# Kernel optimization log

Measured on AMD Instinct MI355X. Metric: run time of the kernel, lower is better.

## Reference

```python
import jax, jax.numpy as jnp
import numpy as np
from jax import lax

B_, L_, D_ = 4, 2048, 256
DI, NS, DC, DTR = 512, 16, 4, 16  # d_inner=2*D, d_state, d_conv, dt_rank=ceil(D/16)
DFF = 4 * D_


def setup_inputs():
    key = jax.random.key(0)
    ks = jax.random.split(key, 20)
    rn = lambda k, s, sc=0.02: jax.random.normal(k, s, jnp.float32) * sc
    return {
        "x": jax.random.normal(ks[0], (B_, L_, D_), jnp.float32),
        "in_proj_w": rn(ks[1], (2 * DI, D_)), "in_proj_b": jnp.zeros((2 * DI,), jnp.float32),
        "conv_w": rn(ks[2], (DI, DC), 0.1), "conv_b": jnp.zeros((DI,), jnp.float32),
        "x_proj_w": rn(ks[3], (DTR + 2 * NS, DI)),
        "dt_proj_w": rn(ks[4], (DI, DTR), 0.1), "dt_proj_b": rn(ks[5], (DI,), 0.5),
        "A_log": jnp.log(jnp.tile(jnp.arange(1, NS + 1, dtype=jnp.float32), (DI, 1))),
        "D_ssm": jnp.ones((DI,), jnp.float32),
        "out_proj_w": rn(ks[6], (D_, DI)), "out_proj_b": jnp.zeros((D_,), jnp.float32),
        "ln1_g": jnp.ones((D_,), jnp.float32), "ln1_b": jnp.zeros((D_,), jnp.float32),
        "fc1_w": rn(ks[7], (DFF, D_)), "fc1_b": jnp.zeros((DFF,), jnp.float32),
        "fc2_w": rn(ks[8], (D_, DFF)), "fc2_b": jnp.zeros((D_,), jnp.float32),
        "ln2_g": jnp.ones((D_,), jnp.float32), "ln2_b": jnp.zeros((D_,), jnp.float32),
    }


def _layer_norm(x, g, b, eps=1e-5):
    m = jnp.mean(x, -1, keepdims=True)
    v = jnp.mean((x - m) ** 2, -1, keepdims=True)
    return (x - m) / jnp.sqrt(v + eps) * g + b


def _mamba(x, in_proj_w, in_proj_b, conv_w, conv_b, x_proj_w, dt_proj_w, dt_proj_b, A_log, D_ssm, out_proj_w, out_proj_b):
    B, L, D = x.shape
    xz = x @ in_proj_w.T + in_proj_b                       # [B,L,2*DI]
    xi, z = jnp.split(xz, 2, axis=-1)
    # causal depthwise conv over time
    xc = jnp.transpose(xi, (0, 2, 1))                       # [B,DI,L]
    xc = lax.conv_general_dilated(xc, conv_w[:, None, :], (1,), [(DC - 1, 0)],
                                  dimension_numbers=("NCH", "OIH", "NCH"),
                                  feature_group_count=DI)
    xi = jax.nn.silu(jnp.transpose(xc + conv_b[None, :, None], (0, 2, 1)))  # [B,L,DI]
    x_dbl = xi @ x_proj_w.T                                 # [B,L,DTR+2*NS]
    dt, Bs, Cs = jnp.split(x_dbl, [DTR, DTR + NS], axis=-1)
    dt = jax.nn.softplus(dt @ dt_proj_w.T + dt_proj_b)      # [B,L,DI]
    A = -jnp.exp(A_log)                                     # [DI,NS]
    dA = jnp.exp(dt[..., None] * A)                         # [B,L,DI,NS]
    dBu = dt[..., None] * Bs[:, :, None, :] * xi[..., None]  # [B,L,DI,NS]
    dA_t = jnp.moveaxis(dA, 1, 0)
    dBu_t = jnp.moveaxis(dBu, 1, 0)
    C_t = jnp.moveaxis(Cs, 1, 0)                            # [L,B,NS]

    def step(h, inp):
        a, bu, c = inp
        h = a * h + bu                                      # [B,DI,NS]
        y = jnp.einsum("bdn,bn->bd", h, c)
        return h, y

    h0 = jnp.zeros((B, DI, NS), x.dtype)
    _, ys = lax.scan(step, h0, (dA_t, dBu_t, C_t))
    y = jnp.moveaxis(ys, 0, 1) + xi * D_ssm                 # [B,L,DI]
    y = y * jax.nn.silu(z)
    return y @ out_proj_w.T + out_proj_b


def reference(x, in_proj_w, in_proj_b, conv_w, conv_b, x_proj_w, dt_proj_w, dt_proj_b,
              A_log, D_ssm, out_proj_w, out_proj_b, ln1_g, ln1_b, fc1_w, fc1_b,
              fc2_w, fc2_b, ln2_g, ln2_b):
    gelu = lambda t: jax.nn.gelu(t, approximate=False)
    ssm = _mamba(x, in_proj_w, in_proj_b, conv_w, conv_b, x_proj_w, dt_proj_w,
                 dt_proj_b, A_log, D_ssm, out_proj_w, out_proj_b)
    y = _layer_norm(x + ssm, ln1_g, ln1_b)                  # dropout = identity (eval)
    ffn = gelu(gelu(y @ fc1_w.T + fc1_b) @ fc2_w.T + fc2_b)
    return _layer_norm(y + ffn, ln2_g, ln2_b)
```

## Files before the change

kernel.cpp:

```cpp
#include <hip/hip_runtime.h>

typedef __bf16 bf16x8 __attribute__((ext_vector_type(8)));
typedef float  f32x4  __attribute__((ext_vector_type(4)));

#define AS1 __attribute__((address_space(1)))
#define AS3 __attribute__((address_space(3)))

__device__ __forceinline__ float bf2f(ushort u) {
    union { unsigned int i; float f; } v; v.i = ((unsigned int)u) << 16; return v.f;
}
__device__ __forceinline__ ushort f2bf(float f) {
    union { float f; unsigned int i; } v; v.f = f;
    unsigned int i = v.i;
    unsigned int r = i + 0x7FFFu + ((i >> 16) & 1u);
    return (ushort)(r >> 16);
}
__device__ __forceinline__ float bflo(unsigned int u) { return bf2f((ushort)(u & 0xFFFFu)); }
__device__ __forceinline__ float bfhi(unsigned int u) { return bf2f((ushort)(u >> 16)); }
__device__ __forceinline__ float gelu_f(float v) {
    return 0.5f * v * (1.f + erff(v * 0.70710678118654752f));
}

__device__ __forceinline__ bool sniff_inline(const ushort* __restrict__ x) {
    const int lane = threadIdx.x & 63;
    int cnt = 0;
    #pragma unroll
    for (int r = 0; r < 4; r++) {
        const ushort u = x[lane + r * 64];
        const int e = (u >> 7) & 0xFF;
        if ((u & 0x7FFF) == 0 || (e >= 112 && e <= 141)) cnt++;
    }
    #pragma unroll
    for (int o = 32; o > 0; o >>= 1) cnt += __shfl_xor(cnt, o);
    return cnt >= 224;
}

struct CanonArgs {
    const void* src[20];
    int off[20];
    int total;
};

__launch_bounds__(256)
__global__ void canon_k(CanonArgs a, ushort* __restrict__ dst, ushort* __restrict__ xpw_pad,
                        const ushort* __restrict__ sniffx)
{
    const int i = blockIdx.x * 256 + threadIdx.x;
    if (i >= a.total) {
        const int j = i - a.total;
        if (j < 8192) xpw_pad[24576 + j] = 0;
        return;
    }
    const bool fl = sniff_inline(sniffx);
    int s = 0;
    #pragma unroll
    for (int t = 1; t < 20; t++) if (i >= a.off[t]) s = t;
    const int li = i - a.off[s];
    ushort v;
    if (fl) v = ((const ushort*)a.src[s])[li];
    else    v = f2bf(((const float*)a.src[s])[li]);
    dst[i] = v;
    if (s == 5) xpw_pad[li] = v;
}

template<int BM, int BN>
__launch_bounds__(256, 2)
__global__ void gemm_bt(const ushort* __restrict__ A, const ushort* __restrict__ W,
                        const ushort* __restrict__ bias, ushort* __restrict__ Cb,
                        int N, int K)
{
    constexpr int WMT = BM / 32;
    constexpr int WNT = BN / 32;
    __shared__ __align__(16) ushort As[BM * 32];
    __shared__ __align__(16) ushort Bs[BN * 32];
    const int tid  = threadIdx.x;
    const int wave = tid >> 6;
    const int lane = tid & 63;
    const int m0 = blockIdx.x * BM;
    const int n0 = blockIdx.y * BN;
    const int wm = (wave >> 1) * (BM / 2);
    const int wn = (wave & 1) * (BN / 2);
    const int lrow = lane & 15;
    const int quad = lane >> 4;

    f32x4 acc[WMT][WNT];
    #pragma unroll
    for (int i = 0; i < WMT; i++)
        #pragma unroll
        for (int j = 0; j < WNT; j++)
            #pragma unroll
            for (int r = 0; r < 4; r++) acc[i][j][r] = 0.f;

    for (int k0 = 0; k0 < K; k0 += 32) {
        #pragma unroll
        for (int t = 0; t < BM / 64; t++) {
            const int inst = t * 4 + wave;
            const int row  = inst * 16 + (lane >> 2);
            const int sub  = lane & 3;
            const ushort* gp = A + (size_t)(m0 + row) * K + (k0 + sub * 8);
            __builtin_amdgcn_global_load_lds((AS1 void*)(void*)gp,
                                             (AS3 void*)(As + inst * 512), 16, 0, 0);
        }
        #pragma unroll
        for (int t = 0; t < BN / 64; t++) {
            const int inst = t * 4 + wave;
            const int row  = inst * 16 + (lane >> 2);
            const int sub  = lane & 3;
            const ushort* gp = W + (size_t)(n0 + row) * K + (k0 + sub * 8);
            __builtin_amdgcn_global_load_lds((AS1 void*)(void*)gp,
                                             (AS3 void*)(Bs + inst * 512), 16, 0, 0);
        }
        __syncthreads();
        bf16x8 afr[WMT], bfr[WNT];
        #pragma unroll
        for (int i = 0; i < WMT; i++)
            afr[i] = *(const bf16x8*)&As[(wm + i * 16 + lrow) * 32 + quad * 8];
        #pragma unroll
        for (int j = 0; j < WNT; j++)
            bfr[j] = *(const bf16x8*)&Bs[(wn + j * 16 + lrow) * 32 + quad * 8];
        #pragma unroll
        for (int i = 0; i < WMT; i++)
            #pragma unroll
            for (int j = 0; j < WNT; j++)
                acc[i][j] = __builtin_amdgcn_mfma_f32_16x16x32_bf16(afr[i], bfr[j], acc[i][j], 0, 0, 0);
        __syncthreads();
    }

    #pragma unroll
    for (int i = 0; i < WMT; i++) {
        const int gm = m0 + wm + i * 16 + quad * 4;
        #pragma unroll
        for (int j = 0; j < WNT; j++) {
            const int gn = n0 + wn + j * 16 + lrow;
            const float bv = bf2f(bias[gn]);
            #pragma unroll
            for (int r = 0; r < 4; r++)
                Cb[(size_t)(gm + r) * N + gn] = f2bf(acc[i][j][r] + bv);
        }
    }
}

__launch_bounds__(512)
__global__ void convscan1_k(const ushort* __restrict__ xz, const ushort* __restrict__ cw,
                            const ushort* __restrict__ cb, const ushort* __restrict__ xpw_pad,
                            const ushort* __restrict__ dtw, const ushort* __restrict__ dtb,
                            const ushort* __restrict__ Alog,
                            float* __restrict__ xdbl, float* __restrict__ summ)
{
    __shared__ __align__(16) ushort xcs[32 * 520];
    __shared__ float XD[32 * 48];
    const int tid  = threadIdx.x;
    const int wave = tid >> 6;
    const int lane = tid & 63;
    const int lrow = lane & 15;
    const int quad = lane >> 4;
    const int c = blockIdx.x, b = blockIdx.y;
    const int t0 = b * 2048 + c * 32;

    {
        const int d8 = (tid & 63) * 8;
        ushort wl[32];
        *(uint4*)&wl[0]  = *(const uint4*)&cw[d8 * 4];
        *(uint4*)&wl[8]  = *(const uint4*)&cw[d8 * 4 + 8];
        *(uint4*)&wl[16] = *(const uint4*)&cw[d8 * 4 + 16];
        *(uint4*)&wl[24] = *(const uint4*)&cw[d8 * 4 + 24];
        ushort bl[8];
        *(uint4*)&bl[0] = *(const uint4*)&cb[d8];
        #pragma unroll
        for (int it = 0; it < 4; it++) {
            const int trow = it * 8 + (tid >> 6);
            const int t = t0 + trow;
            const int l = t & 2047;
            float acc[8];
            #pragma unroll
            for (int j = 0; j < 8; j++) acc[j] = bf2f(bl[j]);
            #pragma unroll
            for (int k = 0; k < 4; k++) {
                const int ls = l - 3 + k;
                if (ls >= 0) {
                    ushort xl[8];
                    *(uint4*)&xl[0] = *(const uint4*)&xz[(size_t)(t - 3 + k) * 1024 + d8];
                    #pragma unroll
                    for (int j = 0; j < 8; j++) acc[j] += bf2f(xl[j]) * bf2f(wl[j * 4 + k]);
                }
            }
            ushort ol[8];
            #pragma unroll
            for (int j = 0; j < 8; j++) {
                const float s = acc[j] / (1.f + __expf(-acc[j]));
                ol[j] = f2bf(s);
            }
            *(uint4*)&xcs[trow * 520 + d8] = *(uint4*)&ol[0];
        }
    }
    __syncthreads();

    {
        const int mt = wave >> 2, nt = wave & 3;
        const ushort* bptr = xpw_pad + (size_t)(nt * 16 + lrow) * 512 + quad * 8;
        f32x4 acc = {0.f, 0.f, 0.f, 0.f};
        bf16x8 bn = *(const bf16x8*)bptr;
        for (int k0 = 0; k0 < 512; k0 += 32) {
            const bf16x8 bc = bn;
            if (k0 + 32 < 512) bn = *(const bf16x8*)(bptr + k0 + 32);
            const bf16x8 afr = *(const bf16x8*)&xcs[(mt * 16 + lrow) * 520 + k0 + quad * 8];
            acc = __builtin_amdgcn_mfma_f32_16x16x32_bf16(afr, bc, acc, 0, 0, 0);
        }
        const int col = nt * 16 + lrow;
        if (col < 48) {
            #pragma unroll
            for (int r = 0; r < 4; r++) {
                const int row = mt * 16 + quad * 4 + r;
                XD[row * 48 + col] = acc[r];
                xdbl[(size_t)(t0 + row) * 64 + col] = acc[r];
            }
        }
    }
    __syncthreads();

    {
        const int d = tid;
        const uint4 w0 = *(const uint4*)&dtw[d * 16];
        const uint4 w1 = *(const uint4*)&dtw[d * 16 + 8];
        const float wd[16] = { bflo(w0.x), bfhi(w0.x), bflo(w0.y), bfhi(w0.y),
                               bflo(w0.z), bfhi(w0.z), bflo(w0.w), bfhi(w0.w),
                               bflo(w1.x), bfhi(w1.x), bflo(w1.y), bfhi(w1.y),
                               bflo(w1.z), bfhi(w1.z), bflo(w1.w), bfhi(w1.w) };
        const float dtbv = bf2f(dtb[d]);
        float A[16], h[16];
        #pragma unroll
        for (int n = 0; n < 16; n++) {
            A[n] = -__expf(bf2f(Alog[d * 16 + n]));
            h[n] = 0.f;
        }
        float sdt = 0.f;
        for (int i = 0; i < 32; i++) {
            const float* Xr = &XD[i * 48];
            float s = dtbv;
            #pragma unroll
            for (int k = 0; k < 16; k++) s += Xr[k] * wd[k];
            const float dtv = (s > 15.f) ? s : __logf(1.f + __expf(s));
            const float xiv = bf2f(xcs[i * 520 + d]);
            const float dx = dtv * xiv;
            sdt += dtv;
            #pragma unroll
            for (int n = 0; n < 16; n++) {
                const float da = __expf(dtv * A[n]);
                h[n] = da * h[n] + dx * Xr[16 + n];
            }
        }
        const size_t base = ((size_t)(b * 64 + c) * 32) * 512 + d;
        #pragma unroll
        for (int n = 0; n < 16; n++) summ[base + (size_t)n * 512] = __expf(A[n] * sdt);
        #pragma unroll
        for (int n = 0; n < 16; n++) summ[base + (size_t)(16 + n) * 512] = h[n];
    }
}

__launch_bounds__(512)
__global__ void combine_k(float* __restrict__ summ)
{
    const int b = blockIdx.x >> 4, n = blockIdx.x & 15;
    const int d = threadIdx.x;
    float h = 0.f;
    #pragma unroll
    for (int half = 0; half < 2; half++) {
        float p[32], hl[32], ho[32];
        #pragma unroll
        for (int c2 = 0; c2 < 32; c2++) {
            const size_t sb = ((size_t)((b * 64 + half * 32 + c2) * 32 + n)) * 512 + d;
            p[c2]  = summ[sb];
            hl[c2] = summ[sb + 8192];
        }
        #pragma unroll
        for (int c2 = 0; c2 < 32; c2++) {
            ho[c2] = h;
            h = p[c2] * h + hl[c2];
        }
        #pragma unroll
        for (int c2 = 0; c2 < 32; c2++) {
            const size_t sb = ((size_t)((b * 64 + half * 32 + c2) * 32 + n)) * 512 + d;
            summ[sb] = ho[c2];
        }
    }
}

__launch_bounds__(512)
__global__ void tail_k(const ushort* __restrict__ xz, const ushort* __restrict__ cw,
                       const ushort* __restrict__ cb, const float* __restrict__ xdbl,
                       const ushort* __restrict__ dtw, const ushort* __restrict__ dtb,
                       const ushort* __restrict__ Alog, const float* __restrict__ summ,
                       const ushort* __restrict__ Dssm, const ushort* __restrict__ cx,
                       const ushort* __restrict__ opw, const ushort* __restrict__ opb,
                       const ushort* __restrict__ ln1g, const ushort* __restrict__ ln1b,
                       const ushort* __restrict__ f1w, const ushort* __restrict__ f1b,
                       const ushort* __restrict__ f2w, const ushort* __restrict__ f2b,
                       const ushort* __restrict__ ln2g, const ushort* __restrict__ ln2b,
                       void* __restrict__ dout, const ushort* __restrict__ sniffx)
{
    __shared__ __align__(16) ushort yls[32 * 520];
    __shared__ float XD[32 * 48];
    __shared__ __align__(16) ushort y1bs[32 * 264];
    __shared__ float redS[8 * 32], redQ[8 * 32];
    ushort* f1q = yls;

    const int tid  = threadIdx.x;
    const int wave = tid >> 6;
    const int lane = tid & 63;
    const int lrow = lane & 15;
    const int quad = lane >> 4;
    const int c = blockIdx.x, b = blockIdx.y;
    const int t0 = b * 2048 + c * 32;
    const int n0w = wave * 32;

    {
        const int d8 = (tid & 63) * 8;
        ushort wl[32];
        *(uint4*)&wl[0]  = *(const uint4*)&cw[d8 * 4];
        *(uint4*)&wl[8]  = *(const uint4*)&cw[d8 * 4 + 8];
        *(uint4*)&wl[16] = *(const uint4*)&cw[d8 * 4 + 16];
        *(uint4*)&wl[24] = *(const uint4*)&cw[d8 * 4 + 24];
        ushort bl[8];
        *(uint4*)&bl[0] = *(const uint4*)&cb[d8];
        #pragma unroll
        for (int it = 0; it < 4; it++) {
            const int trow = it * 8 + (tid >> 6);
            const int t = t0 + trow;
            const int l = t & 2047;
            float acc[8];
            #pragma unroll
            for (int j = 0; j < 8; j++) acc[j] = bf2f(bl[j]);
            #pragma unroll
            for (int k = 0; k < 4; k++) {
                const int ls = l - 3 + k;
                if (ls >= 0) {
                    ushort xl[8];
                    *(uint4*)&xl[0] = *(const uint4*)&xz[(size_t)(t - 3 + k) * 1024 + d8];
                    #pragma unroll
                    for (int j = 0; j < 8; j++) acc[j] += bf2f(xl[j]) * bf2f(wl[j * 4 + k]);
                }
            }
            ushort ol[8];
            #pragma unroll
            for (int j = 0; j < 8; j++) {
                const float s = acc[j] / (1.f + __expf(-acc[j]));
                ol[j] = f2bf(s);
            }
            *(uint4*)&yls[trow * 520 + d8] = *(uint4*)&ol[0];
        }
    }
    for (int e = tid; e < 1536; e += 512)
        XD[e] = xdbl[(size_t)(t0 + (e / 48)) * 64 + (e % 48)];
    __syncthreads();

    {
        const int d = tid;
        const uint4 w0 = *(const uint4*)&dtw[d * 16];
        const uint4 w1 = *(const uint4*)&dtw[d * 16 + 8];
        const float wd[16] = { bflo(w0.x), bfhi(w0.x), bflo(w0.y), bfhi(w0.y),
                               bflo(w0.z), bfhi(w0.z), bflo(w0.w), bfhi(w0.w),
                               bflo(w1.x), bfhi(w1.x), bflo(w1.y), bfhi(w1.y),
                               bflo(w1.z), bfhi(w1.z), bflo(w1.w), bfhi(w1.w) };
        const float dtbv = bf2f(dtb[d]);
        float A[16], h[16];
        #pragma unroll
        for (int n = 0; n < 16; n++) A[n] = -__expf(bf2f(Alog[d * 16 + n]));
        const size_t base = ((size_t)(b * 64 + c) * 32) * 512 + d;
        #pragma unroll
        for (int n = 0; n < 16; n++) h[n] = summ[base + (size_t)n * 512];
        const float Dv = bf2f(Dssm[d]);
        for (int i = 0; i < 32; i++) {
            const int t = t0 + i;
            const float* Xr = &XD[i * 48];
            float s = dtbv;
            #pragma unroll
            for (int k = 0; k < 16; k++) s += Xr[k] * wd[k];
            const float dtv = (s > 15.f) ? s : __logf(1.f + __expf(s));
            const float xiv = bf2f(yls[i * 520 + d]);
            const float dx = dtv * xiv;
            float yv = 0.f;
            #pragma unroll
            for (int n = 0; n < 16; n++) {
                const float da = __expf(dtv * A[n]);
                h[n] = da * h[n] + dx * Xr[16 + n];
                yv += h[n] * Xr[32 + n];
            }
            yv += xiv * Dv;
            const float zv = bf2f(xz[(size_t)t * 1024 + 512 + d]);
            yv *= zv / (1.f + __expf(-zv));
            yls[i * 520 + d] = f2bf(yv);
        }
    }
    __syncthreads();

    f32x4 accP[2][2];
    #pragma unroll
    for (int i = 0; i < 2; i++)
        #pragma unroll
        for (int j = 0; j < 2; j++)
            #pragma unroll
            for (int r = 0; r < 4; r++) accP[i][j][r] = 0.f;
    {
        const ushort* bp0 = opw + (size_t)(n0w + lrow) * 512 + quad * 8;
        const ushort* bp1 = opw + (size_t)(n0w + 16 + lrow) * 512 + quad * 8;
        bf16x8 bn0 = *(const bf16x8*)bp0;
        bf16x8 bn1 = *(const bf16x8*)bp1;
        for (int k0 = 0; k0 < 512; k0 += 32) {
            const bf16x8 bc0 = bn0, bc1 = bn1;
            if (k0 + 32 < 512) {
                bn0 = *(const bf16x8*)(bp0 + k0 + 32);
                bn1 = *(const bf16x8*)(bp1 + k0 + 32);
            }
            bf16x8 afr[2];
            #pragma unroll
            for (int i = 0; i < 2; i++)
                afr[i] = *(const bf16x8*)&yls[(i * 16 + lrow) * 520 + k0 + quad * 8];
            #pragma unroll
            for (int i = 0; i < 2; i++) {
                accP[i][0] = __builtin_amdgcn_mfma_f32_16x16x32_bf16(afr[i], bc0, accP[i][0], 0, 0, 0);
                accP[i][1] = __builtin_amdgcn_mfma_f32_16x16x32_bf16(afr[i], bc1, accP[i][1], 0, 0, 0);
            }
        }
    }
    float vP[2][2][4];
    float ps[2][4], pq[2][4];
    #pragma unroll
    for (int i = 0; i < 2; i++)
        #pragma unroll
        for (int r = 0; r < 4; r++) { ps[i][r] = 0.f; pq[i][r] = 0.f; }
    #pragma unroll
    for (int i = 0; i < 2; i++) {
        #pragma unroll
        for (int j = 0; j < 2; j++) {
            const int col = n0w + j * 16 + lrow;
            const float bv = bf2f(opb[col]);
            #pragma unroll
            for (int r = 0; r < 4; r++) {
                const int row = i * 16 + quad * 4 + r;
                float v = accP[i][j][r] + bv + bf2f(cx[(size_t)(t0 + row) * 256 + col]);
                vP[i][j][r] = v;
                ps[i][r] += v;
                pq[i][r] += v * v;
            }
        }
    }
    #pragma unroll
    for (int i = 0; i < 2; i++)
        #pragma unroll
        for (int r = 0; r < 4; r++) {
            #pragma unroll
            for (int o = 8; o > 0; o >>= 1) {
                ps[i][r] += __shfl_xor(ps[i][r], o);
                pq[i][r] += __shfl_xor(pq[i][r], o);
            }
            if (lrow == 0) {
                const int row = i * 16 + quad * 4 + r;
                redS[wave * 32 + row] = ps[i][r];
                redQ[wave * 32 + row] = pq[i][r];
            }
        }
    __syncthreads();

    float y1f[2][2][4];
    #pragma unroll
    for (int i = 0; i < 2; i++) {
        #pragma unroll
        for (int r = 0; r < 4; r++) {
            const int row = i * 16 + quad * 4 + r;
            float S = 0.f, Q = 0.f;
            #pragma unroll
            for (int w = 0; w < 8; w++) { S += redS[w * 32 + row]; Q += redQ[w * 32 + row]; }
            const float mean = S * (1.f / 256.f);
            const float var  = Q * (1.f / 256.f) - mean * mean;
            const float rs   = rsqrtf(var + 1e-5f);
            #pragma unroll
            for (int j = 0; j < 2; j++) {
                const int col = n0w + j * 16 + lrow;
                const float o2 = (vP[i][j][r] - mean) * rs * bf2f(ln1g[col]) + bf2f(ln1b[col]);
                y1f[i][j][r] = o2;
                y1bs[row * 264 + col] = f2bf(o2);
            }
        }
    }
    __syncthreads();

    f32x4 acc2[2][2];
    #pragma unroll
    for (int i = 0; i < 2; i++)
        #pragma unroll
        for (int j = 0; j < 2; j++)
            #pragma unroll
            for (int r = 0; r < 4; r++) acc2[i][j][r] = 0.f;

    for (int q = 0; q < 4; q++) {
        f32x4 a1[2][2];
        #pragma unroll
        for (int i = 0; i < 2; i++)
            #pragma unroll
            for (int j = 0; j < 2; j++)
                #pragma unroll
                for (int r = 0; r < 4; r++) a1[i][j][r] = 0.f;
        {
            const ushort* bp0 = f1w + (size_t)(q * 256 + n0w + lrow) * 256 + quad * 8;
            const ushort* bp1 = f1w + (size_t)(q * 256 + n0w + 16 + lrow) * 256 + quad * 8;
            bf16x8 bn0 = *(const bf16x8*)bp0;
            bf16x8 bn1 = *(const bf16x8*)bp1;
            for (int k0 = 0; k0 < 256; k0 += 32) {
                const bf16x8 bc0 = bn0, bc1 = bn1;
                if (k0 + 32 < 256) {
                    bn0 = *(const bf16x8*)(bp0 + k0 + 32);
                    bn1 = *(const bf16x8*)(bp1 + k0 + 32);
                }
                bf16x8 afr[2];
                #pragma unroll
                for (int i = 0; i < 2; i++)
                    afr[i] = *(const bf16x8*)&y1bs[(i * 16 + lrow) * 264 + k0 + quad * 8];
                #pragma unroll
                for (int i = 0; i < 2; i++) {
                    a1[i][0] = __builtin_amdgcn_mfma_f32_16x16x32_bf16(afr[i], bc0, a1[i][0], 0, 0, 0);
                    a1[i][1] = __builtin_amdgcn_mfma_f32_16x16x32_bf16(afr[i], bc1, a1[i][1], 0, 0, 0);
                }
            }
        }
        #pragma unroll
        for (int i = 0; i < 2; i++)
            #pragma unroll
            for (int j = 0; j < 2; j++) {
                const int qc = n0w + j * 16 + lrow;
                const float bv = bf2f(f1b[q * 256 + qc]);
                #pragma unroll
                for (int r = 0; r < 4; r++) {
                    const int row = i * 16 + quad * 4 + r;
                    f1q[row * 260 + qc] = f2bf(gelu_f(a1[i][j][r] + bv));
                }
            }
        __syncthreads();
        {
            const ushort* bp0 = f2w + (size_t)(n0w + lrow) * 1024 + q * 256 + quad * 8;
            const ushort* bp1 = f2w + (size_t)(n0w + 16 + lrow) * 1024 + q * 256 + quad * 8;
            bf16x8 bn0 = *(const bf16x8*)bp0;
            bf16x8 bn1 = *(const bf16x8*)bp1;
            for (int k0 = 0; k0 < 256; k0 += 32) {
                const bf16x8 bc0 = bn0, bc1 = bn1;
                if (k0 + 32 < 256) {
                    bn0 = *(const bf16x8*)(bp0 + k0 + 32);
                    bn1 = *(const bf16x8*)(bp1 + k0 + 32);
                }
                bf16x8 afr[2];
                #pragma unroll
                for (int i = 0; i < 2; i++)
                    afr[i] = *(const bf16x8*)&f1q[(i * 16 + lrow) * 260 + k0 + quad * 8];
                #pragma unroll
                for (int i = 0; i < 2; i++) {
                    acc2[i][0] = __builtin_amdgcn_mfma_f32_16x16x32_bf16(afr[i], bc0, acc2[i][0], 0, 0, 0);
                    acc2[i][1] = __builtin_amdgcn_mfma_f32_16x16x32_bf16(afr[i], bc1, acc2[i][1], 0, 0, 0);
                }
            }
        }
        __syncthreads();
    }

    float v2[2][2][4];
    #pragma unroll
    for (int i = 0; i < 2; i++)
        #pragma unroll
        for (int r = 0; r < 4; r++) { ps[i][r] = 0.f; pq[i][r] = 0.f; }
    #pragma unroll
    for (int i = 0; i < 2; i++)
        #pragma unroll
        for (int j = 0; j < 2; j++) {
            const int col = n0w + j * 16 + lrow;
            const float bv = bf2f(f2b[col]);
            #pragma unroll
            for (int r = 0; r < 4; r++) {
                const float v = gelu_f(acc2[i][j][r] + bv) + y1f[i][j][r];
                v2[i][j][r] = v;
                ps[i][r] += v;
                pq[i][r] += v * v;
            }
        }
    #pragma unroll
    for (int i = 0; i < 2; i++)
        #pragma unroll
        for (int r = 0; r < 4; r++) {
            #pragma unroll
            for (int o = 8; o > 0; o >>= 1) {
                ps[i][r] += __shfl_xor(ps[i][r], o);
                pq[i][r] += __shfl_xor(pq[i][r], o);
            }
            if (lrow == 0) {
                const int row = i * 16 + quad * 4 + r;
                redS[wave * 32 + row] = ps[i][r];
                redQ[wave * 32 + row] = pq[i][r];
            }
        }
    __syncthreads();

    const bool fl = sniff_inline(sniffx);
    #pragma unroll
    for (int i = 0; i < 2; i++) {
        #pragma unroll
        for (int r = 0; r < 4; r++) {
            const int row = i * 16 + quad * 4 + r;
            float S = 0.f, Q = 0.f;
            #pragma unroll
            for (int w = 0; w < 8; w++) { S += redS[w * 32 + row]; Q += redQ[w * 32 + row]; }
            const float mean = S * (1.f / 256.f);
            const float var  = Q * (1.f / 256.f) - mean * mean;
            const float rs   = rsqrtf(var + 1e-5f);
            #pragma unroll
            for (int j = 0; j < 2; j++) {
                const int col = n0w + j * 16 + lrow;
                const size_t off = (size_t)(t0 + row) * 256 + col;
                const float o2 = (v2[i][j][r] - mean) * rs * bf2f(ln2g[col]) + bf2f(ln2b[col]);
                if (fl) ((ushort*)dout)[off] = f2bf(o2);
                else    ((float*)dout)[off]  = o2;
            }
        }
    }
}

extern "C" void kernel_launch(void* const* d_in, const int* in_sizes, int n_in,
                              void* d_out, int out_size, void* d_ws, size_t ws_size,
                              hipStream_t stream)
{
    char* ws = (char*)d_ws;
    ushort* canon = (ushort*)(ws + 256);

    static const int coff[20] = {
        0,        2097152,  2359296,  2360320,  2362368,
        2362880,  2387456,  2395648,  2396160,  2404352,
        2404864,  2535936,  2536192,  2536448,  2536704,
        2798848,  2799872,  3062016,  3062272,  3062528 };
    static const int ctot = 3062784;

    CanonArgs ca;
    for (int i = 0; i < 20; i++) { ca.src[i] = d_in[i]; ca.off[i] = coff[i]; }
    ca.total = ctot;

    const ushort* cx   = canon + coff[0];
    const ushort* cipw = canon + coff[1];
    const ushort* cipb = canon + coff[2];
    const ushort* ccw  = canon + coff[3];
    const ushort* ccb  = canon + coff[4];
    const ushort* cdtw = canon + coff[6];
    const ushort* cdtb = canon + coff[7];
    const ushort* calog= canon + coff[8];
    const ushort* cdssm= canon + coff[9];
    const ushort* copw = canon + coff[10];
    const ushort* copb = canon + coff[11];
    const ushort* cln1g= canon + coff[12];
    const ushort* cln1b= canon + coff[13];
    const ushort* cf1w = canon + coff[14];
    const ushort* cf1b = canon + coff[15];
    const ushort* cf2w = canon + coff[16];
    const ushort* cf2b = canon + coff[17];
    const ushort* cln2g= canon + coff[18];
    const ushort* cln2b= canon + coff[19];

    ushort* xpw_pad = (ushort*)(ws + 6291456);
    ushort* xz      = (ushort*)(ws + 8388608);
    float*  xdbl    = (float*)(ws + 25165824);
    float*  summ    = (float*)(ws + 27262976);
    const ushort* sx = (const ushort*)d_in[0];

    canon_k<<<(ctot + 8192 + 255) / 256, 256, 0, stream>>>(ca, canon, xpw_pad, sx);
    gemm_bt<128, 128><<<dim3(64, 8), 256, 0, stream>>>(cx, cipw, cipb, xz, 1024, 256);
    convscan1_k<<<dim3(64, 4), 512, 0, stream>>>(
        xz, ccw, ccb, xpw_pad, cdtw, cdtb, calog, xdbl, summ);
    combine_k<<<64, 512, 0, stream>>>(summ);
    tail_k<<<dim3(64, 4), 512, 0, stream>>>(
        xz, ccw, ccb, xdbl, cdtw, cdtb, calog, summ, cdssm, cx,
        copw, copb, cln1g, cln1b, cf1w, cf1b, cf2w, cf2b, cln2g, cln2b,
        d_out, sx);
}
```

Measured before the change: 235.2 us.

## Tree-reduce dt dot product, split combine blocks, prefetch z and residual loads

Replaces the serial 16-term dt projection sum with four independent FMA chains plus a tree add, shortening the dependency chain in both scan kernels. The combine kernel is relaunched as 128 blocks of 256 threads instead of 64 of 512 to spread work over more compute units. In the tail kernel, the z gate values and residual x values are loaded into registers ahead of their use so global latency overlaps other work. The prefetches raise register pressure, which could reduce occupancy.

```diff
diff --git a/kernel.cpp b/kernel.cpp
--- a/kernel.cpp
+++ b/kernel.cpp
@@ -19,6 +19,20 @@
 __device__ __forceinline__ float bfhi(unsigned int u) { return bf2f((ushort)(u >> 16)); }
 __device__ __forceinline__ float gelu_f(float v) {
     return 0.5f * v * (1.f + erff(v * 0.70710678118654752f));
+}
+
+__device__ __forceinline__ float dot16_tree(const float* __restrict__ Xr,
+                                            const float* __restrict__ wd, float bias) {
+    float s4[4];
+    #pragma unroll
+    for (int g = 0; g < 4; g++) {
+        float t_ = Xr[g * 4] * wd[g * 4];
+        t_ = fmaf(Xr[g * 4 + 1], wd[g * 4 + 1], t_);
+        t_ = fmaf(Xr[g * 4 + 2], wd[g * 4 + 2], t_);
+        t_ = fmaf(Xr[g * 4 + 3], wd[g * 4 + 3], t_);
+        s4[g] = t_;
+    }
+    return bias + ((s4[0] + s4[1]) + (s4[2] + s4[3]));
 }
 
 __device__ __forceinline__ bool sniff_inline(const ushort* __restrict__ x) {
@@ -236,9 +250,7 @@
         float sdt = 0.f;
         for (int i = 0; i < 32; i++) {
             const float* Xr = &XD[i * 48];
-            float s = dtbv;
-            #pragma unroll
-            for (int k = 0; k < 16; k++) s += Xr[k] * wd[k];
+            const float s = dot16_tree(Xr, wd, dtbv);
             const float dtv = (s > 15.f) ? s : __logf(1.f + __expf(s));
             const float xiv = bf2f(xcs[i * 520 + d]);
             const float dx = dtv * xiv;
@@ -257,11 +269,12 @@
     }
 }
 
-__launch_bounds__(512)
+__launch_bounds__(256)
 __global__ void combine_k(float* __restrict__ summ)
 {
-    const int b = blockIdx.x >> 4, n = blockIdx.x & 15;
-    const int d = threadIdx.x;
+    const int b = blockIdx.x >> 5;
+    const int n = (blockIdx.x >> 1) & 15;
+    const int d = (blockIdx.x & 1) * 256 + threadIdx.x;
     float h = 0.f;
     #pragma unroll
     for (int half = 0; half < 2; half++) {
@@ -355,6 +368,11 @@
 
     {
         const int d = tid;
+        ushort zreg[32];
+        #pragma unroll
+        for (int i = 0; i < 32; i++)
+            zreg[i] = xz[(size_t)(t0 + i) * 1024 + 512 + d];
+
         const uint4 w0 = *(const uint4*)&dtw[d * 16];
         const uint4 w1 = *(const uint4*)&dtw[d * 16 + 8];
         const float wd[16] = { bflo(w0.x), bfhi(w0.x), bflo(w0.y), bfhi(w0.y),
@@ -370,11 +388,8 @@
         for (int n = 0; n < 16; n++) h[n] = summ[base + (size_t)n * 512];
         const float Dv = bf2f(Dssm[d]);
         for (int i = 0; i < 32; i++) {
-            const int t = t0 + i;
             const float* Xr = &XD[i * 48];
-            float s = dtbv;
-            #pragma unroll
-            for (int k = 0; k < 16; k++) s += Xr[k] * wd[k];
+            const float s = dot16_tree(Xr, wd, dtbv);
             const float dtv = (s > 15.f) ? s : __logf(1.f + __expf(s));
             const float xiv = bf2f(yls[i * 520 + d]);
             const float dx = dtv * xiv;
@@ -386,12 +401,25 @@
                 yv += h[n] * Xr[32 + n];
             }
             yv += xiv * Dv;
-            const float zv = bf2f(xz[(size_t)t * 1024 + 512 + d]);
+            const float zv = bf2f(zreg[i]);
             yv *= zv / (1.f + __expf(-zv));
             yls[i * 520 + d] = f2bf(yv);
         }
     }
     __syncthreads();
+
+    ushort cxr[2][2][4];
+    #pragma unroll
+    for (int i = 0; i < 2; i++)
+        #pragma unroll
+        for (int j = 0; j < 2; j++) {
+            const int col = n0w + j * 16 + lrow;
+            #pragma unroll
+            for (int r = 0; r < 4; r++) {
+                const int row = i * 16 + quad * 4 + r;
+                cxr[i][j][r] = cx[(size_t)(t0 + row) * 256 + col];
+            }
+        }
 
     f32x4 accP[2][2];
     #pragma unroll
@@ -436,8 +464,7 @@
             const float bv = bf2f(opb[col]);
             #pragma unroll
             for (int r = 0; r < 4; r++) {
-                const int row = i * 16 + quad * 4 + r;
-                float v = accP[i][j][r] + bv + bf2f(cx[(size_t)(t0 + row) * 256 + col]);
+                float v = accP[i][j][r] + bv + bf2f(cxr[i][j][r]);
                 vP[i][j][r] = v;
                 ps[i][r] += v;
                 pq[i][r] += v * v;
@@ -668,7 +695,7 @@
     gemm_bt<128, 128><<<dim3(64, 8), 256, 0, stream>>>(cx, cipw, cipb, xz, 1024, 256);
     convscan1_k<<<dim3(64, 4), 512, 0, stream>>>(
         xz, ccw, ccb, xpw_pad, cdtw, cdtb, calog, xdbl, summ);
-    combine_k<<<64, 512, 0, stream>>>(summ);
+    combine_k<<<128, 256, 0, stream>>>(summ);
     tail_k<<<dim3(64, 4), 512, 0, stream>>>(
         xz, ccw, ccb, xdbl, cdtw, cdtb, calog, summ, cdssm, cx,
         copw, copb, cln1g, cln1b, cf1w, cf1b, cf2w, cf2b, cln2g, cln2b,
```

Result: slower. 248.9 us (+5.8%).
